# Kernel optimization log

Measured on AMD Instinct MI355X. Metric: run time of the kernel, lower is better.

The kernel has to match this reference:

```python
import jax, jax.numpy as jnp
import numpy as np

NFFT = 512
HOP = 256
N_FREQ = NFFT // 2


def _imdct_kernels():
    # Matches _get_imdct_kernels: windowed IMDCT cosine basis, shape [nfft, nfft//2]
    def kernel_fn(time, freq):
        win = np.sin(np.pi * (2 * time + 1) / (2.0 * NFFT))
        return np.cos(np.pi / NFFT * (2 * time + 1 + NFFT / 2.0) * (freq + 0.5)) * win
    k = np.fromfunction(kernel_fn, (NFFT, N_FREQ), dtype=np.float64)
    return jnp.asarray(k.astype(np.float32))  # [nfft, n_freq]


def setup_inputs() -> dict:
    key = jax.random.key(0)
    spec = jax.random.normal(key, (16, 1, N_FREQ, 4096), dtype=jnp.float32)
    return {"spec": spec, "kernels": _imdct_kernels()}


def reference(spec, kernels):
    # spec: [B, 1, n_freq, T]; kernels: [nfft, n_freq]
    B, _, _, T = spec.shape
    # conv2d with (n_freq,1) kernel == per-frame basis matmul over frequency
    frames = jnp.einsum('bft,kf->btk', spec[:, 0], kernels) * (4.0 / NFFT)  # [B, T, nfft]
    # conv_transpose2d with identity-diagonal kernel and stride=hop == overlap-add
    L = (T - 1) * HOP + NFFT
    idx = jnp.arange(T)[:, None] * HOP + jnp.arange(NFFT)[None, :]  # [T, nfft]
    out = jnp.zeros((B, L), dtype=spec.dtype).at[:, idx].add(frames)
    return out
```

## Files before the change

kernel.cpp:

```cpp
#include <hip/hip_runtime.h>
#include <stdint.h>

#define NFREQ 256
#define NB 16
#define NT 4096
#define LOUT 1048832
#define TROWS 65
#define TROW 132

typedef __bf16 bf16;
typedef __bf16 bf16x8 __attribute__((ext_vector_type(8)));
typedef float floatx4 __attribute__((ext_vector_type(4)));

__device__ inline uint32_t f_as_u(float x) { union { float f; uint32_t u; } v; v.f = x; return v.u; }
__device__ inline uint32_t bf16r(float x) {
    uint32_t u = f_as_u(x);
    return (u + 0x7fffu + ((u >> 16) & 1u)) >> 16;
}

__global__ __launch_bounds__(256) void build_kb(const float* __restrict__ ker,
                                                bf16* __restrict__ kbF) {
    int idx = blockIdx.x * 256 + threadIdx.x;
    int n = idx >> 9, f = idx & 511;
    float v = (f < 256) ? ker[(n + 256) * 256 + f] : ker[n * 256 + (f - 256)];
    uint32_t rr = bf16r(v * 0.0078125f);
    union { uint16_t u; bf16 b; } o; o.u = (uint16_t)rr;
    kbF[((size_t)(f >> 5) * 256 + n) * 32 + (f & 31)] = o.b;
}

#define STAGE_GROUP(TtB, J0, rb) { \
    float v_[16]; \
    _Pragma("unroll") \
    for (int i_ = 0; i_ < 16; ++i_) { \
        int r_ = (rb) * 16 + i_; int tc_ = r_ >> 5, fpi_ = r_ & 31; \
        int f_ = (fpw + fpi_) * 2 + lpar; \
        int t_ = (J0) - 1 + tc_ * 32 + lt; \
        v_[i_] = ((unsigned)t_ < (unsigned)NT) ? sb[(size_t)f_ * NT + t_] : 0.0f; } \
    _Pragma("unroll") \
    for (int i_ = 0; i_ < 16; i_ += 2) { \
        int r_ = (rb) * 16 + i_; int tc_ = r_ >> 5, fpi_ = r_ & 31; \
        int tl_ = tc_ * 32 + lt; \
        uint32_t h0_ = bf16r(v_[i_]);     uint32_t o0_ = (uint32_t)__shfl_xor((int)h0_, 1); \
        uint32_t h1_ = bf16r(v_[i_ + 1]); uint32_t o1_ = (uint32_t)__shfl_xor((int)h1_, 1); \
        if (lpar == 0) { \
            uint2 pk_; pk_.x = (h0_ & 0xffffu) | (o0_ << 16); pk_.y = (h1_ & 0xffffu) | (o1_ << 16); \
            *reinterpret_cast<uint2*>(&(TtB)[tl_ * TROW + fpw + fpi_]) = pk_; } } }

#define STAGE_ROW64(TtB, J0) { \
    int f_ = w * 64 + lane; int te_ = (J0) + 63; \
    float v_ = ((unsigned)te_ < (unsigned)NT) ? sb[(size_t)f_ * NT + te_] : 0.0f; \
    uint32_t h_ = bf16r(v_); uint32_t o_ = (uint32_t)__shfl_xor((int)h_, 1); \
    if (lpar == 0) (TtB)[64 * TROW + w * 32 + lt] = (h_ & 0xffffu) | (o_ << 16); }

#define LOADB(dst, kc) { \
    _Pragma("unroll") \
    for (int jn_ = 0; jn_ < 4; ++jn_) \
        dst[jn_] = *reinterpret_cast<const bf16x8*>( \
            kbw + (size_t)(kc) * 8192 + (jn_ * 16 + row16) * 32 + q * 8); }

#define LOADA(dst, Tb, kki, ks) { \
    _Pragma("unroll") \
    for (int i_ = 0; i_ < 4; ++i_) \
        dst[i_] = *reinterpret_cast<const bf16x8*>( \
            (Tb) + (size_t)(i_ * 16 + row16 + ((kki) >= 4 ? 1 : 0)) * 528 \
                 + ((kki) & 3) * 128 + (ks) * 64 + q * 16); }

#define DOMFMA(af_, bf_) { \
    _Pragma("unroll") \
    for (int i_ = 0; i_ < 4; ++i_) \
        _Pragma("unroll") \
        for (int jn_ = 0; jn_ < 4; ++jn_) \
            acc[i_][jn_] = __builtin_amdgcn_mfma_f32_16x16x32_bf16(af_[i_], bf_[jn_], acc[i_][jn_], 0, 0, 0); }

#define STORE_TILE(J0) { \
    _Pragma("unroll") \
    for (int i_ = 0; i_ < 4; ++i_) { \
        _Pragma("unroll") \
        for (int e_ = 0; e_ < 4; ++e_) { \
            int j_ = (J0) + i_ * 16 + q * 4 + e_; \
            if (j_ <= 4096) { \
                float* orow_ = out + (size_t)b * LOUT + (size_t)j_ * 256 + w * 64; \
                _Pragma("unroll") \
                for (int jn_ = 0; jn_ < 4; ++jn_) \
                    orow_[jn_ * 16 + row16] = acc[i_][jn_][e_]; } } } }

__global__ __launch_bounds__(256, 2) void imdct_gemm(const float* __restrict__ spec,
                                                     const bf16* __restrict__ kbF,
                                                     float* __restrict__ out) {
    __shared__ uint32_t Tt[2][TROWS * TROW];

    const int b  = blockIdx.y;
    const int tid = threadIdx.x, lane = tid & 63, w = tid >> 6;
    const int j0t0 = blockIdx.x * 128;
    const int j0t1 = j0t0 + 64;
    const bool has1 = (blockIdx.x < 32);
    const float* sb = spec + (size_t)b * NFREQ * NT;

    const int lpar = lane & 1, lt = lane >> 1;
    const int fpw = w * 32;
    const int row16 = lane & 15, q = lane >> 4;
    const bf16* kbw = kbF + (size_t)w * 64 * 32;
    uint32_t* Tt0 = &Tt[0][0];
    uint32_t* Tt1 = &Tt[1][0];

    STAGE_GROUP(Tt0, j0t0, 0);
    STAGE_GROUP(Tt0, j0t0, 1);
    STAGE_GROUP(Tt0, j0t0, 2);
    STAGE_GROUP(Tt0, j0t0, 3);
    STAGE_ROW64(Tt0, j0t0);
    __syncthreads();

    floatx4 acc[4][4] = {};
    {
        const uint8_t* Tb = reinterpret_cast<const uint8_t*>(Tt0);
        #pragma unroll
        for (int kki = 0; kki < 8; ++kki) {
            if (has1) {
                if (kki == 0) STAGE_GROUP(Tt1, j0t1, 0);
                if (kki == 1) STAGE_GROUP(Tt1, j0t1, 1);
                if (kki == 2) STAGE_GROUP(Tt1, j0t1, 2);
                if (kki == 3) STAGE_GROUP(Tt1, j0t1, 3);
                if (kki == 4) STAGE_ROW64(Tt1, j0t1);
            }
            bf16x8 af[4], bfr[4];
            LOADB(bfr, kki * 2 + 0);
            LOADA(af, Tb, kki, 0);
            DOMFMA(af, bfr);
            LOADB(bfr, kki * 2 + 1);
            LOADA(af, Tb, kki, 1);
            DOMFMA(af, bfr);
        }
    }
    __syncthreads();

    STORE_TILE(j0t0);

    if (has1) {
        #pragma unroll
        for (int i = 0; i < 4; ++i)
            #pragma unroll
            for (int jn = 0; jn < 4; ++jn)
                acc[i][jn] = (floatx4){0.f, 0.f, 0.f, 0.f};
        const uint8_t* Tb = reinterpret_cast<const uint8_t*>(Tt1);
        #pragma unroll
        for (int kki = 0; kki < 8; ++kki) {
            bf16x8 af[4], bfr[4];
            LOADB(bfr, kki * 2 + 0);
            LOADA(af, Tb, kki, 0);
            DOMFMA(af, bfr);
            LOADB(bfr, kki * 2 + 1);
            LOADA(af, Tb, kki, 1);
            DOMFMA(af, bfr);
        }
        STORE_TILE(j0t1);
    }
}

extern "C" void kernel_launch(void* const* d_in, const int* in_sizes, int n_in,
                              void* d_out, int out_size, void* d_ws, size_t ws_size,
                              hipStream_t stream) {
    const float* spec = (const float*)d_in[0];
    const float* ker  = (const float*)d_in[1];
    float* out = (float*)d_out;

    bf16* kbF = (bf16*)d_ws;

    build_kb<<<512, 256, 0, stream>>>(ker, kbF);
    imdct_gemm<<<dim3(33, NB), 256, 0, stream>>>(spec, kbF, out);
}
```

Baseline: 145.5 us.

## Issue all second-tile global loads before first tile MFMA and prefetch B fragments

The staging of the second time tile is split into an issue phase that loads all 65 values per thread into registers and a later pack phase that converts and writes them to LDS. All second-tile global loads are issued before the first tile's MFMA loop, so their latency overlaps that compute. The B-fragment loads are double-buffered so the next chunk is fetched while the current MFMAs run. The cost is about 65 extra live float registers plus more B buffers, which under launch_bounds(256,2) may raise register pressure or cause spills.

```diff
diff --git a/kernel.cpp b/kernel.cpp
--- a/kernel.cpp
+++ b/kernel.cpp
@@ -28,42 +28,40 @@
     kbF[((size_t)(f >> 5) * 256 + n) * 32 + (f & 31)] = o.b;
 }
 
-#define STAGE_GROUP(TtB, J0, rb) { \
-    float v_[16]; \
+#define STAGE_ISSUE(J0) { \
     _Pragma("unroll") \
-    for (int i_ = 0; i_ < 16; ++i_) { \
-        int r_ = (rb) * 16 + i_; int tc_ = r_ >> 5, fpi_ = r_ & 31; \
+    for (int r_ = 0; r_ < 64; ++r_) { \
+        int tc_ = r_ >> 5, fpi_ = r_ & 31; \
         int f_ = (fpw + fpi_) * 2 + lpar; \
         int t_ = (J0) - 1 + tc_ * 32 + lt; \
-        v_[i_] = ((unsigned)t_ < (unsigned)NT) ? sb[(size_t)f_ * NT + t_] : 0.0f; } \
+        vs_[r_] = ((unsigned)t_ < (unsigned)NT) ? sb[(size_t)f_ * NT + t_] : 0.0f; } \
+    { int f_ = w * 64 + lane; int te_ = (J0) + 63; \
+      vs_[64] = ((unsigned)te_ < (unsigned)NT) ? sb[(size_t)f_ * NT + te_] : 0.0f; } }
+
+#define STAGE_PACK(TtB) { \
     _Pragma("unroll") \
-    for (int i_ = 0; i_ < 16; i_ += 2) { \
-        int r_ = (rb) * 16 + i_; int tc_ = r_ >> 5, fpi_ = r_ & 31; \
+    for (int r_ = 0; r_ < 64; r_ += 2) { \
+        int tc_ = r_ >> 5, fpi_ = r_ & 31; \
         int tl_ = tc_ * 32 + lt; \
-        uint32_t h0_ = bf16r(v_[i_]);     uint32_t o0_ = (uint32_t)__shfl_xor((int)h0_, 1); \
-        uint32_t h1_ = bf16r(v_[i_ + 1]); uint32_t o1_ = (uint32_t)__shfl_xor((int)h1_, 1); \
+        uint32_t h0_ = bf16r(vs_[r_]);     uint32_t o0_ = (uint32_t)__shfl_xor((int)h0_, 1); \
+        uint32_t h1_ = bf16r(vs_[r_ + 1]); uint32_t o1_ = (uint32_t)__shfl_xor((int)h1_, 1); \
         if (lpar == 0) { \
             uint2 pk_; pk_.x = (h0_ & 0xffffu) | (o0_ << 16); pk_.y = (h1_ & 0xffffu) | (o1_ << 16); \
-            *reinterpret_cast<uint2*>(&(TtB)[tl_ * TROW + fpw + fpi_]) = pk_; } } }
+            *reinterpret_cast<uint2*>(&(TtB)[tl_ * TROW + fpw + fpi_]) = pk_; } } \
+    { uint32_t h_ = bf16r(vs_[64]); uint32_t o_ = (uint32_t)__shfl_xor((int)h_, 1); \
+      if (lpar == 0) (TtB)[64 * TROW + w * 32 + lt] = (h_ & 0xffffu) | (o_ << 16); } }
 
-#define STAGE_ROW64(TtB, J0) { \
-    int f_ = w * 64 + lane; int te_ = (J0) + 63; \
-    float v_ = ((unsigned)te_ < (unsigned)NT) ? sb[(size_t)f_ * NT + te_] : 0.0f; \
-    uint32_t h_ = bf16r(v_); uint32_t o_ = (uint32_t)__shfl_xor((int)h_, 1); \
-    if (lpar == 0) (TtB)[64 * TROW + w * 32 + lt] = (h_ & 0xffffu) | (o_ << 16); }
-
-#define LOADB(dst, kc) { \
+#define LOADB(dst, c) { \
     _Pragma("unroll") \
     for (int jn_ = 0; jn_ < 4; ++jn_) \
         dst[jn_] = *reinterpret_cast<const bf16x8*>( \
-            kbw + (size_t)(kc) * 8192 + (jn_ * 16 + row16) * 32 + q * 8); }
+            kbw + (size_t)(c) * 8192 + (jn_ * 16 + row16) * 32 + q * 8); }
 
-#define LOADA(dst, Tb, kki, ks) { \
+#define LOADA(dst, Tb, c) { \
     _Pragma("unroll") \
     for (int i_ = 0; i_ < 4; ++i_) \
         dst[i_] = *reinterpret_cast<const bf16x8*>( \
-            (Tb) + (size_t)(i_ * 16 + row16 + ((kki) >= 4 ? 1 : 0)) * 528 \
-                 + ((kki) & 3) * 128 + (ks) * 64 + q * 16); }
+            (Tb) + (size_t)(i_ * 16 + row16 + ((c) >> 3)) * 528 + ((c) & 7) * 64 + q * 16); }
 
 #define DOMFMA(af_, bf_) { \
     _Pragma("unroll") \
@@ -71,6 +69,20 @@
         _Pragma("unroll") \
         for (int jn_ = 0; jn_ < 4; ++jn_) \
             acc[i_][jn_] = __builtin_amdgcn_mfma_f32_16x16x32_bf16(af_[i_], bf_[jn_], acc[i_][jn_], 0, 0, 0); }
+
+#define COMPUTE_TILE(TtB) { \
+    const uint8_t* Tb_ = reinterpret_cast<const uint8_t*>(TtB); \
+    bf16x8 bP[4], bQ[4], af[4]; \
+    LOADB(bP, 0); \
+    _Pragma("unroll") \
+    for (int cc = 0; cc < 8; ++cc) { \
+        LOADB(bQ, cc * 2 + 1); \
+        LOADA(af, Tb_, cc * 2); \
+        DOMFMA(af, bP); \
+        if (cc < 7) LOADB(bP, cc * 2 + 2); \
+        LOADA(af, Tb_, cc * 2 + 1); \
+        DOMFMA(af, bQ); \
+    } }
 
 #define STORE_TILE(J0) { \
     _Pragma("unroll") \
@@ -103,56 +115,30 @@
     uint32_t* Tt0 = &Tt[0][0];
     uint32_t* Tt1 = &Tt[1][0];
 
-    STAGE_GROUP(Tt0, j0t0, 0);
-    STAGE_GROUP(Tt0, j0t0, 1);
-    STAGE_GROUP(Tt0, j0t0, 2);
-    STAGE_GROUP(Tt0, j0t0, 3);
-    STAGE_ROW64(Tt0, j0t0);
+    float vs_[65];
+    floatx4 acc[4][4] = {};
+
+    STAGE_ISSUE(j0t0);
+    STAGE_PACK(Tt0);
     __syncthreads();
 
-    floatx4 acc[4][4] = {};
-    {
-        const uint8_t* Tb = reinterpret_cast<const uint8_t*>(Tt0);
-        #pragma unroll
-        for (int kki = 0; kki < 8; ++kki) {
-            if (has1) {
-                if (kki == 0) STAGE_GROUP(Tt1, j0t1, 0);
-                if (kki == 1) STAGE_GROUP(Tt1, j0t1, 1);
-                if (kki == 2) STAGE_GROUP(Tt1, j0t1, 2);
-                if (kki == 3) STAGE_GROUP(Tt1, j0t1, 3);
-                if (kki == 4) STAGE_ROW64(Tt1, j0t1);
-            }
-            bf16x8 af[4], bfr[4];
-            LOADB(bfr, kki * 2 + 0);
-            LOADA(af, Tb, kki, 0);
-            DOMFMA(af, bfr);
-            LOADB(bfr, kki * 2 + 1);
-            LOADA(af, Tb, kki, 1);
-            DOMFMA(af, bfr);
-        }
-    }
-    __syncthreads();
+    if (has1) { STAGE_ISSUE(j0t1); }
 
-    STORE_TILE(j0t0);
+    COMPUTE_TILE(Tt0);
 
     if (has1) {
+        STAGE_PACK(Tt1);
+        __syncthreads();
+        STORE_TILE(j0t0);
         #pragma unroll
         for (int i = 0; i < 4; ++i)
             #pragma unroll
             for (int jn = 0; jn < 4; ++jn)
                 acc[i][jn] = (floatx4){0.f, 0.f, 0.f, 0.f};
-        const uint8_t* Tb = reinterpret_cast<const uint8_t*>(Tt1);
-        #pragma unroll
-        for (int kki = 0; kki < 8; ++kki) {
-            bf16x8 af[4], bfr[4];
-            LOADB(bfr, kki * 2 + 0);
-            LOADA(af, Tb, kki, 0);
-            DOMFMA(af, bfr);
-            LOADB(bfr, kki * 2 + 1);
-            LOADA(af, Tb, kki, 1);
-            DOMFMA(af, bfr);
-        }
+        COMPUTE_TILE(Tt1);
         STORE_TILE(j0t1);
+    } else {
+        STORE_TILE(j0t0);
     }
 }
 
```

After: 142.7 us. 2.0% less time.
